# Kernel tuning notes

Measured on AMD Instinct MI355X. Metric: run time of the kernel, lower is better.

Reference implementation:

```python
import jax, jax.numpy as jnp
import numpy as np

# __init__ hyperparameters (defaults)
TRACE_BINS = 24
SMOOTH_KERNEL = 5
PAUSE_ENERGY_STD = -0.5
PAUSE_DELTA_Q = 0.35
VOICED_STD = -0.1
BOUNDARY_Q = 0.75

B, T, MEL = 64, 8000, 80


def _sliding_mean(x, k):
    """avg_pool1d(stride=1, padding=k//2, count_include_pad=True) via cumsum. x: [B,T]."""
    pad = k // 2
    xp = jnp.pad(x, ((0, 0), (pad, pad)))
    c = jnp.pad(jnp.cumsum(xp, axis=1), ((0, 0), (1, 0)))
    return (c[:, k:] - c[:, :-k]) / k


def _run_mean(mask):
    """Mean length of runs of True in mask [B,T] = (#ones)/(#runs), 0 if no runs."""
    prev_off = jnp.pad(~mask[:, :-1], ((0, 0), (1, 0)), constant_values=True)
    starts = mask & prev_off
    n_runs = starts.sum(axis=1).astype(jnp.float32)
    ones = mask.sum(axis=1).astype(jnp.float32)
    return jnp.where(n_runs > 0, ones / jnp.maximum(n_runs, 1.0), 0.0)


def setup_inputs() -> dict:
    key = jax.random.key(0)
    ref_mel = jax.random.normal(key, (B, T, MEL), dtype=jnp.float32)
    return {"ref_mel": ref_mel}


def reference(ref_mel):
    b, t, _ = ref_mel.shape
    energy = ref_mel.mean(axis=-1)                                  # [B,T]
    mu = energy.mean(axis=1, keepdims=True)
    sd = jnp.maximum(energy.std(axis=1, keepdims=True, ddof=1), 1e-6)  # torch.std is unbiased
    z = (energy - mu) / sd

    delta = jnp.pad(jnp.abs(energy[:, 1:] - energy[:, :-1]), ((0, 0), (1, 0)))
    dthr = jnp.quantile(delta, PAUSE_DELTA_Q, axis=1, keepdims=True)
    pause = (z <= PAUSE_ENERGY_STD) & (delta <= dthr)
    speech = ~pause
    voiced = (z > VOICED_STD).astype(jnp.float32)

    k = min(SMOOTH_KERNEL, max(1, t))
    local_rate = _sliding_mean(delta, k)[:, :t]
    k2 = min(k + 2, max(1, t))
    boundary_strength = _sliding_mean(delta, k2)[:, :t]

    sp = jnp.cumsum(speech.astype(jnp.float32), axis=1)
    total = jnp.maximum(sp[:, -1:], 1.0)
    progress = sp / total                                           # [B,T], nondecreasing
    uniform = jnp.linspace(0.0, 1.0, t)[None, :]
    seg_bias = progress - uniform

    bthr = jnp.quantile(boundary_strength, BOUNDARY_Q, axis=1, keepdims=True)
    bev = (boundary_strength >= bthr).astype(jnp.float32)

    feat = jnp.stack([pause.astype(jnp.float32), local_rate, bev, seg_bias, voiced], axis=-1)  # [B,T,5]

    # progress-based resampling: parallel binary search + gather + lerp
    target = jnp.linspace(0.0, 1.0, TRACE_BINS)
    right = jax.vmap(lambda p: jnp.searchsorted(p, target, side='left'))(progress)  # [B,bins]
    left = jnp.clip(right - 1, 0, t - 1)
    rc = jnp.clip(right, 0, t - 1)
    pl = jnp.take_along_axis(progress, left, axis=1)
    pr = jnp.take_along_axis(progress, rc, axis=1)
    denom = jnp.maximum(jnp.abs(pr - pl), 1e-6)
    alpha = jnp.clip((target[None, :] - pl) / denom, 0.0, 1.0)
    alpha = jnp.where(right <= 0, 0.0, jnp.where(right >= t, 1.0, alpha))[..., None]  # [B,bins,1]
    fdim = feat.shape[-1]
    li = jnp.broadcast_to(left[:, :, None], (b, TRACE_BINS, fdim))
    ri = jnp.broadcast_to(rc[:, :, None], (b, TRACE_BINS, fdim))
    fl = jnp.take_along_axis(feat, li, axis=1)
    fr = jnp.take_along_axis(feat, ri, axis=1)
    trace = fl * (1.0 - alpha) + fr * alpha                          # [B,bins,5]

    stats = jnp.stack([
        pause.astype(jnp.float32).mean(axis=1),
        _run_mean(pause),
        _run_mean(speech),
        local_rate[:, -1] - local_rate[:, 0],
        bev.mean(axis=1),
        voiced.mean(axis=1),
    ], axis=-1)                                                      # [B,6]
    return stats, trace
```

## Files before the change

### kernel.cpp

```cpp
#include <hip/hip_runtime.h>
#include <hip/hip_bf16.h>

#define TT 8000
#define BB 64
#define NBINS 24
#define CAP 256
#define NT 1024
#define NS 8
#define NHB 1024

__global__ __launch_bounds__(256) void k_energy(const float* __restrict__ mel,
                                                double* __restrict__ e_bt){
  __shared__ float sm[5120];
  const int blk = blockIdx.x, tid = threadIdx.x;
  const float4* g = (const float4*)(mel + (size_t)blk * 5120);
  float4* s4 = (float4*)sm;
  #pragma unroll
  for (int j = 0; j < 5; ++j) s4[tid + j * 256] = g[tid + j * 256];
  __syncthreads();
  const float* p = sm + tid * 20;
  double s = 0.0;
  #pragma unroll
  for (int j = 0; j < 20; ++j) s += (double)p[j];
  s += __shfl_xor(s, 1, 64);
  s += __shfl_xor(s, 2, 64);
  if ((tid & 3) == 0) e_bt[(size_t)blk * 64 + (tid >> 2)] = s / 80.0;
}

#define FALLBACK(VALS, RNK, OUTLO, MAXV, CBASE)                                  \
  {                                                                              \
    double lo_ = -0.5, hi_ = (MAXV);                                             \
    int cl_ = 0, ch_ = 8000;                                                     \
    for (;;){                                                                    \
      if (ch_ - cl_ <= CAP){                                                     \
        if (tid == 0) redI[0] = 0;                                               \
        __syncthreads();                                                         \
        _Pragma("unroll")                                                        \
        for (int s = 0; s < NS; ++s){                                            \
          int t = tid + (s << 10);                                               \
          if (t < TT){ double v = VALS[s];                                       \
            if (v > lo_ && v <= hi_){ int ix = atomicAdd(&redI[0], 1);           \
              if (ix < CAP) cand[(CBASE) + ix] = v; } }                          \
        }                                                                        \
        __syncthreads();                                                         \
        int n = redI[0]; if (n > CAP) n = CAP;                                   \
        int tgt = (RNK) - cl_;                                                   \
        if (tid < n){                                                            \
          double mv = cand[(CBASE) + tid];                                       \
          int rk = 0;                                                            \
          for (int j = 0; j < n; ++j){ double cj = cand[(CBASE) + j];            \
            rk += (cj < mv || (cj == mv && j < tid)) ? 1 : 0; }                  \
          if (rk == tgt)     scD[OUTLO] = mv;                                    \
          if (rk == tgt + 1) scD[(OUTLO) + 1] = mv;                              \
        }                                                                        \
        __syncthreads();                                                         \
        break;                                                                   \
      }                                                                          \
      double mid_ = 0.5 * (lo_ + hi_);                                           \
      if (!(mid_ > lo_ && mid_ < hi_)){                                          \
        if (tid == 0){ scD[OUTLO] = hi_; scD[(OUTLO) + 1] = hi_; }               \
        __syncthreads();                                                         \
        break;                                                                   \
      }                                                                          \
      int c_ = 0;                                                                \
      _Pragma("unroll")                                                          \
      for (int s = 0; s < NS; ++s){                                              \
        int t = tid + (s << 10);                                                 \
        if (t < TT && VALS[s] <= mid_) c_++;                                     \
      }                                                                          \
      _Pragma("unroll")                                                          \
      for (int o = 32; o; o >>= 1) c_ += __shfl_down(c_, o, 64);                 \
      if (lane == 0) redI[wid] = c_;                                             \
      __syncthreads();                                                           \
      if (tid == 0){ int a2 = 0; for (int i = 0; i < 16; ++i) a2 += redI[i]; scI[5] = a2; } \
      __syncthreads();                                                           \
      int ct_ = scI[5];                                                          \
      if (ct_ <= (RNK)){ lo_ = mid_; cl_ = ct_; }                                \
      else if (ct_ >= (RNK) + 2){ hi_ = mid_; ch_ = ct_; }                       \
      else {                                                                     \
        double mx_ = -1.0, mn_ = 1e300;                                          \
        _Pragma("unroll")                                                        \
        for (int s = 0; s < NS; ++s){                                            \
          int t = tid + (s << 10);                                               \
          if (t < TT){ double v = VALS[s];                                       \
            if (v <= mid_){ if (v > mx_) mx_ = v; } else { if (v < mn_) mn_ = v; } } \
        }                                                                        \
        _Pragma("unroll")                                                        \
        for (int o = 32; o; o >>= 1){ double x = __shfl_down(mx_, o, 64); if (x > mx_) mx_ = x; } \
        if (lane == 0) redD[wid] = mx_;                                          \
        __syncthreads();                                                         \
        if (tid == 0){ double a2 = redD[0]; for (int i = 1; i < 16; ++i) if (redD[i] > a2) a2 = redD[i]; scD[OUTLO] = a2; } \
        __syncthreads();                                                         \
        _Pragma("unroll")                                                        \
        for (int o = 32; o; o >>= 1){ double x = __shfl_down(mn_, o, 64); if (x < mn_) mn_ = x; } \
        if (lane == 0) redD[wid] = mn_;                                          \
        __syncthreads();                                                         \
        if (tid == 0){ double a2 = redD[0]; for (int i = 1; i < 16; ++i) if (redD[i] < a2) a2 = redD[i]; scD[(OUTLO) + 1] = a2; } \
        __syncthreads();                                                         \
        break;                                                                   \
      }                                                                          \
    }                                                                            \
  }

__global__ __launch_bounds__(NT) void k_row(const double* __restrict__ e_all,
                                            float* __restrict__ out){
  __shared__ double e_s[TT];
  __shared__ double delta_s[TT];
  __shared__ __align__(16) unsigned short runs[TT];
  __shared__ unsigned char flags[TT];
  __shared__ double cand[2 * CAP];
  __shared__ double redD[64];
  __shared__ int    redI[16];
  __shared__ double scD[12];
  __shared__ int    scI[16];
  __shared__ int    wTD[16], wOD[16], wTB[16], wOB[16], wT[16], wO[16];
  __shared__ int    cnt5[5];
  int* histD = (int*)runs;
  int* histB = histD + NHB;

  const int b = blockIdx.x, tid = threadIdx.x;
  const int lane = tid & 63, wid = tid >> 6;
  const double* eg = e_all + (size_t)b * TT;

  if (tid < 5) cnt5[tid] = 0;
  if (tid < 16) scI[tid] = 0;
  histD[tid] = 0; histB[tid] = 0;

  double ev[NS], dv[NS], bv[NS];
  #pragma unroll
  for (int s = 0; s < NS; ++s){
    int t = tid + (s << 10);
    double e = (t < TT) ? eg[t] : 0.0;
    ev[s] = e;
    if (t < TT) e_s[t] = e;
  }
  __syncthreads();
  #pragma unroll
  for (int s = 0; s < NS; ++s){
    int t = tid + (s << 10);
    double d = 0.0;
    if (t > 0 && t < TT) d = fabs(e_s[t] - e_s[t-1]);
    dv[s] = d;
    if (t < TT) delta_s[t] = d;
  }
  __syncthreads();
  #pragma unroll
  for (int s = 0; s < NS; ++s){
    int t = tid + (s << 10);
    double sum = 0.0;
    if (t < TT){
      int j0 = t - 3; if (j0 < 0) j0 = 0;
      int j1 = t + 3; if (j1 > TT-1) j1 = TT-1;
      for (int j = j0; j <= j1; ++j) sum += delta_s[j];
    }
    bv[s] = sum / 7.0;
  }
  {
    double se = 0.0, s2 = 0.0, md = 0.0, mb = 0.0;
    #pragma unroll
    for (int s = 0; s < NS; ++s){
      se += ev[s]; s2 += ev[s] * ev[s];
      if (dv[s] > md) md = dv[s];
      if (bv[s] > mb) mb = bv[s];
    }
    #pragma unroll
    for (int o = 32; o; o >>= 1){
      se += __shfl_down(se, o, 64);
      s2 += __shfl_down(s2, o, 64);
      double x = __shfl_down(md, o, 64); if (x > md) md = x;
      x = __shfl_down(mb, o, 64); if (x > mb) mb = x;
    }
    if (lane == 0){ redD[wid] = se; redD[16+wid] = s2; redD[32+wid] = md; redD[48+wid] = mb; }
  }
  __syncthreads();
  if (tid < 64){
    double a = (lane < 16) ? redD[lane]      : 0.0;
    double q = (lane < 16) ? redD[16 + lane] : 0.0;
    double c = (lane < 16) ? redD[32 + lane] : 0.0;
    double d = (lane < 16) ? redD[48 + lane] : 0.0;
    #pragma unroll
    for (int o = 8; o; o >>= 1){
      a += __shfl_down(a, o, 64);
      q += __shfl_down(q, o, 64);
      double x = __shfl_down(c, o, 64); if (x > c) c = x;
      x = __shfl_down(d, o, 64); if (x > d) d = x;
    }
    if (lane == 0){
      double mu0 = a / 8000.0;
      double var = (q - a * a / 8000.0) / 7999.0;
      if (var < 0.0) var = 0.0;
      double sd0 = sqrt(var); if (sd0 < 1e-6) sd0 = 1e-6;
      scD[0] = mu0; scD[1] = sd0; scD[9] = c; scD[10] = d;
    }
  }
  __syncthreads();
  const double mu = scD[0], sd = scD[1];
  const double maxd = scD[9], maxb = scD[10];
  const bool doD = (maxd > 0.0), doB = (maxb > 0.0);
  const double sclD = doD ? (double)NHB / maxd : 0.0;
  const double sclB = doB ? (double)NHB / maxb : 0.0;
  #pragma unroll
  for (int s = 0; s < NS; ++s){
    int t = tid + (s << 10);
    if (t < TT){
      if (doD){ int bi = (int)(dv[s] * sclD); if (bi > NHB-1) bi = NHB-1; atomicAdd(&histD[bi], 1); }
      if (doB){ int bi = (int)(bv[s] * sclB); if (bi > NHB-1) bi = NHB-1; atomicAdd(&histB[bi], 1); }
    }
  }
  __syncthreads();
  const int hD = histD[tid], hB = histB[tid];
  int incD = hD, incB = hB;
  #pragma unroll
  for (int o = 1; o < 64; o <<= 1){
    int x = __shfl_up(incD, o, 64); if (lane >= o) incD += x;
    x = __shfl_up(incB, o, 64); if (lane >= o) incB += x;
  }
  if (lane == 63){ wTD[wid] = incD; wTB[wid] = incB; }
  __syncthreads();
  if (tid < 64){
    int vD = (lane < 16) ? wTD[lane] : 0;
    int vB = (lane < 16) ? wTB[lane] : 0;
    int iD = vD, iB = vB;
    #pragma unroll
    for (int o = 1; o < 16; o <<= 1){
      int x = __shfl_up(iD, o, 64); if (lane >= o) iD += x;
      x = __shfl_up(iB, o, 64); if (lane >= o) iB += x;
    }
    if (lane < 16){ wOD[lane] = iD - vD; wOB[lane] = iB - vB; }
  }
  __syncthreads();
  {
    int PD = wOD[wid] + incD;
    int PB = wOB[wid] + incB;
    if (doD){
      if (2799 >= PD - hD && 2799 < PD){ scI[0] = tid; scI[2] = PD - hD; }
      if (2800 >= PD - hD && 2800 < PD){ scI[1] = tid; scI[3] = PD; }
    }
    if (doB){
      if (5999 >= PB - hB && 5999 < PB){ scI[8]  = tid; scI[10] = PB - hB; }
      if (6000 >= PB - hB && 6000 < PB){ scI[9]  = tid; scI[11] = PB; }
    }
  }
  __syncthreads();
  const int binrD = scI[0], binr1D = scI[1], PmD = scI[2], cwinD = scI[3] - scI[2];
  const int binrB = scI[8], binr1B = scI[9], PmB = scI[10], cwinB = scI[11] - scI[10];
  const bool fastD = doD && (cwinD <= CAP);
  const bool fastB = doB && (cwinB <= CAP);
  #pragma unroll
  for (int s = 0; s < NS; ++s){
    int t = tid + (s << 10);
    if (t < TT){
      if (fastD){
        int bi = (int)(dv[s] * sclD); if (bi > NHB-1) bi = NHB-1;
        if (bi >= binrD && bi <= binr1D){ int ix = atomicAdd(&scI[4], 1); if (ix < CAP) cand[ix] = dv[s]; }
      }
      if (fastB){
        int bi = (int)(bv[s] * sclB); if (bi > NHB-1) bi = NHB-1;
        if (bi >= binrB && bi <= binr1B){ int ix = atomicAdd(&scI[12], 1); if (ix < CAP) cand[CAP + ix] = bv[s]; }
      }
    }
  }
  __syncthreads();
  if (fastD){
    int n = scI[4]; if (n > CAP) n = CAP;
    int tgt = 2799 - PmD;
    if (tid < n){
      double mv = cand[tid];
      int rk = 0;
      for (int j = 0; j < n; ++j){ double cj = cand[j]; rk += (cj < mv || (cj == mv && j < tid)) ? 1 : 0; }
      if (rk == tgt)     scD[4] = mv;
      if (rk == tgt + 1) scD[5] = mv;
    }
  }
  if (fastB){
    int n = scI[12]; if (n > CAP) n = CAP;
    int tgt = 5999 - PmB;
    if (tid < n){
      double mv = cand[CAP + tid];
      int rk = 0;
      for (int j = 0; j < n; ++j){ double cj = cand[CAP + j]; rk += (cj < mv || (cj == mv && j < tid)) ? 1 : 0; }
      if (rk == tgt)     scD[6] = mv;
      if (rk == tgt + 1) scD[7] = mv;
    }
  }
  __syncthreads();
  if (doD && !fastD){ FALLBACK(dv, 2799, 4, maxd, 0) }
  if (doB && !fastB){ FALLBACK(bv, 5999, 6, maxb, CAP) }
  if (tid == 0){
    double gD = 0.35 * 7999.0 - 2799.0;
    double dd = scD[5] - scD[4];
    scD[2] = doD ? ((gD >= 0.5) ? (scD[5] - dd * (1.0 - gD)) : (scD[4] + dd * gD)) : 0.0;
    double gB = 0.75 * 7999.0 - 5999.0;
    double db = scD[7] - scD[6];
    scD[3] = doB ? ((gB >= 0.5) ? (scD[7] - db * (1.0 - gB)) : (scD[6] + db * gB)) : 0.0;
  }
  __syncthreads();
  const double dthr = scD[2], bthr = scD[3];
  #pragma unroll
  for (int s = 0; s < NS; ++s){
    int t = tid + (s << 10);
    if (t < TT){
      double z = (ev[s] - mu) / sd;
      bool pause  = (z <= -0.5) && (dv[s] <= dthr);
      bool voiced = (z > -0.1);
      bool bev    = (bv[s] >= bthr);
      flags[t] = (unsigned char)((pause ? 1 : 0) | (voiced ? 2 : 0) | (bev ? 4 : 0));
    }
  }
  __syncthreads();
  {
    int cp = 0, crp = 0, crs = 0, cv = 0, cb = 0;
    #pragma unroll
    for (int s = 0; s < NS; ++s){
      int t = tid + (s << 10);
      if (t < TT){
        unsigned f = flags[t];
        bool pause = (f & 1) != 0;
        bool prevP = (t > 0) ? ((flags[t-1] & 1) != 0) : false;
        cp += pause ? 1 : 0; cv += (f >> 1) & 1; cb += (f >> 2) & 1;
        if (pause && (t == 0 || !prevP)) crp++;
        if (!pause && (t == 0 || prevP)) crs++;
      }
    }
    #pragma unroll
    for (int o = 32; o; o >>= 1){
      cp += __shfl_down(cp, o, 64); crp += __shfl_down(crp, o, 64);
      crs += __shfl_down(crs, o, 64); cv += __shfl_down(cv, o, 64);
      cb += __shfl_down(cb, o, 64);
    }
    if (lane == 0){
      atomicAdd(&cnt5[0], cp); atomicAdd(&cnt5[1], crp); atomicAdd(&cnt5[2], crs);
      atomicAdd(&cnt5[3], cv); atomicAdd(&cnt5[4], cb);
    }
  }
  const int t0 = tid * 8;
  int ls = 0;
  if (t0 < TT){
    #pragma unroll
    for (int k = 0; k < 8; ++k) ls += (flags[t0 + k] & 1) ? 0 : 1;
  }
  int inc = ls;
  #pragma unroll
  for (int o = 1; o < 64; o <<= 1){ int x = __shfl_up(inc, o, 64); if (lane >= o) inc += x; }
  if (lane == 63) wT[wid] = inc;
  __syncthreads();
  if (tid < 64){
    int v = (lane < 16) ? wT[lane] : 0;
    int i2 = v;
    #pragma unroll
    for (int o = 1; o < 16; o <<= 1){ int x = __shfl_up(i2, o, 64); if (lane >= o) i2 += x; }
    if (lane < 16) wO[lane] = i2 - v;
    if (lane == 15) scD[8] = (i2 > 1) ? (double)i2 : 1.0;
  }
  __syncthreads();
  const double tf = scD[8];
  if (t0 < TT){
    int run = wO[wid] + (inc - ls);
    #pragma unroll
    for (int k = 0; k < 8; ++k){
      int t = t0 + k;
      run += (flags[t] & 1) ? 0 : 1;
      runs[t] = (unsigned short)run;
    }
  }
  __syncthreads();
  if (tid == 0){
    float onesP = (float)cnt5[0];
    float onesS = (float)(TT - cnt5[0]);
    float* st = out + b * 6;
    st[0] = onesP / 8000.0f;
    st[1] = (cnt5[1] > 0) ? (onesP / fmaxf((float)cnt5[1], 1.0f)) : 0.0f;
    st[2] = (cnt5[2] > 0) ? (onesS / fmaxf((float)cnt5[2], 1.0f)) : 0.0f;
    st[3] = (float)((delta_s[7997] + delta_s[7998] + delta_s[7999]) / 5.0
                  - (delta_s[0] + delta_s[1] + delta_s[2]) / 5.0);
    st[4] = ((float)cnt5[4]) / 8000.0f;
    st[5] = ((float)cnt5[3]) / 8000.0f;
  }
  if (tid < NBINS){
    double target = (tid == NBINS - 1) ? 1.0 : (double)tid * (1.0 / 23.0);
    int lo2 = 0, hi2 = TT;
    while (lo2 < hi2){
      int mid = (lo2 + hi2) >> 1;
      if ((double)runs[mid] / tf < target) lo2 = mid + 1; else hi2 = mid;
    }
    int right = lo2;
    int li = right - 1; if (li < 0) li = 0; if (li > TT-1) li = TT-1;
    int ri = right;     if (ri < 0) ri = 0; if (ri > TT-1) ri = TT-1;
    double pl = (double)runs[li] / tf, pr = (double)runs[ri] / tf;
    double denom = fabs(pr - pl); if (denom < 1e-6) denom = 1e-6;
    double alpha = (target - pl) / denom;
    if (alpha < 0.0) alpha = 0.0;
    if (alpha > 1.0) alpha = 1.0;
    if (right <= 0) alpha = 0.0;
    else if (right >= TT) alpha = 1.0;
    double fL[5], fR[5];
    for (int sdx = 0; sdx < 2; ++sdx){
      int i = sdx ? ri : li;
      double* f = sdx ? fR : fL;
      unsigned fl = flags[i];
      int j0 = i - 2; if (j0 < 0) j0 = 0;
      int j1 = i + 2; if (j1 > TT-1) j1 = TT-1;
      double ws = 0.0;
      for (int j = j0; j <= j1; ++j) ws += delta_s[j];
      f[0] = (fl & 1) ? 1.0 : 0.0;
      f[1] = ws / 5.0;
      f[2] = (fl & 4) ? 1.0 : 0.0;
      double u = (i == TT - 1) ? 1.0 : (double)i * (1.0 / 7999.0);
      f[3] = (double)runs[i] / tf - u;
      f[4] = (fl & 2) ? 1.0 : 0.0;
    }
    double om = 1.0 - alpha;
    float* tr = out + BB * 6 + ((size_t)b * NBINS + tid) * 5;
    #pragma unroll
    for (int f = 0; f < 5; ++f)
      tr[f] = (float)(fL[f] * om + fR[f] * alpha);
  }
}

extern "C" void kernel_launch(void* const* d_in, const int* in_sizes, int n_in,
                              void* d_out, int out_size, void* d_ws, size_t ws_size,
                              hipStream_t stream){
  const float* mel = (const float*)d_in[0];
  float* out = (float*)d_out;
  double* e_bt = (double*)d_ws;

  hipLaunchKernelGGL(k_energy, dim3(8000), dim3(256), 0, stream, mel, e_bt);
  hipLaunchKernelGGL(k_row,    dim3(BB),   dim3(NT),  0, stream, e_bt, out);
}
```

Baseline: 51.70 us.

## Use fixed histogram scale and cut block barriers in per-row quantile kernel

Replaces the data-dependent histogram scale, which needed a block-wide max reduction and barrier first, with a fixed scale of 1024. This lets histogram building run in the same pass as the mean/variance accumulation. Several __syncthreads and small scan stages are removed: neighbour deltas come from wavefront shuffles, previous-pause flags come from bitmasks, and per-wave prefix offsets are summed redundantly by each thread. The risk is that a fixed scale clusters values into few bins, which would push more rows into the slower fallback selection path (that path now computes its own max).

Measured after the change: 51.22 us, median of 2. No clear change (-0.9%).

```diff
diff --git a/kernel.cpp b/kernel.cpp
--- a/kernel.cpp
+++ b/kernel.cpp
@@ -8,6 +8,7 @@
 #define NT 1024
 #define NS 8
 #define NHB 1024
+#define FSCALE 1024.0
 
 __global__ __launch_bounds__(256) void k_energy(const float* __restrict__ mel,
                                                 double* __restrict__ e_bt){
@@ -27,9 +28,21 @@
   if ((tid & 3) == 0) e_bt[(size_t)blk * 64 + (tid >> 2)] = s / 80.0;
 }
 
-#define FALLBACK(VALS, RNK, OUTLO, MAXV, CBASE)                                  \
+#define FALLBACK(VALS, RNK, OUTLO, CBASE)                                        \
   {                                                                              \
-    double lo_ = -0.5, hi_ = (MAXV);                                             \
+    double mx0 = 0.0;                                                            \
+    _Pragma("unroll")                                                            \
+    for (int s = 0; s < NS; ++s){                                                \
+      int t = tid + (s << 10);                                                   \
+      if (t < TT && VALS[s] > mx0) mx0 = VALS[s];                                \
+    }                                                                            \
+    _Pragma("unroll")                                                            \
+    for (int o = 32; o; o >>= 1){ double x = __shfl_down(mx0, o, 64); if (x > mx0) mx0 = x; } \
+    if (lane == 0) redD[wid] = mx0;                                              \
+    __syncthreads();                                                             \
+    if (tid == 0){ double a2 = redD[0]; for (int i = 1; i < 16; ++i) if (redD[i] > a2) a2 = redD[i]; scD[11] = a2; } \
+    __syncthreads();                                                             \
+    double lo_ = -0.5, hi_ = scD[11];                                            \
     int cl_ = 0, ch_ = 8000;                                                     \
     for (;;){                                                                    \
       if (ch_ - cl_ <= CAP){                                                     \
@@ -109,11 +122,11 @@
   __shared__ __align__(16) unsigned short runs[TT];
   __shared__ unsigned char flags[TT];
   __shared__ double cand[2 * CAP];
-  __shared__ double redD[64];
+  __shared__ double redD[32];
   __shared__ int    redI[16];
   __shared__ double scD[12];
   __shared__ int    scI[16];
-  __shared__ int    wTD[16], wOD[16], wTB[16], wOB[16], wT[16], wO[16];
+  __shared__ int    wTD[16], wTB[16], wT[16];
   __shared__ int    cnt5[5];
   int* histD = (int*)runs;
   int* histB = histD + NHB;
@@ -134,128 +147,87 @@
     ev[s] = e;
     if (t < TT) e_s[t] = e;
   }
-  __syncthreads();
   #pragma unroll
   for (int s = 0; s < NS; ++s){
     int t = tid + (s << 10);
-    double d = 0.0;
-    if (t > 0 && t < TT) d = fabs(e_s[t] - e_s[t-1]);
+    double ep = __shfl_up(ev[s], 1, 64);
+    if (lane == 0 && t > 0 && t < TT) ep = eg[t - 1];
+    double d = (t > 0 && t < TT) ? fabs(ev[s] - ep) : 0.0;
     dv[s] = d;
     if (t < TT) delta_s[t] = d;
   }
   __syncthreads();
-  #pragma unroll
-  for (int s = 0; s < NS; ++s){
-    int t = tid + (s << 10);
-    double sum = 0.0;
-    if (t < TT){
-      int j0 = t - 3; if (j0 < 0) j0 = 0;
-      int j1 = t + 3; if (j1 > TT-1) j1 = TT-1;
-      for (int j = j0; j <= j1; ++j) sum += delta_s[j];
-    }
-    bv[s] = sum / 7.0;
-  }
   {
-    double se = 0.0, s2 = 0.0, md = 0.0, mb = 0.0;
+    double se = 0.0, s2 = 0.0;
     #pragma unroll
     for (int s = 0; s < NS; ++s){
-      se += ev[s]; s2 += ev[s] * ev[s];
-      if (dv[s] > md) md = dv[s];
-      if (bv[s] > mb) mb = bv[s];
-    }
-    #pragma unroll
-    for (int o = 32; o; o >>= 1){
-      se += __shfl_down(se, o, 64);
-      s2 += __shfl_down(s2, o, 64);
-      double x = __shfl_down(md, o, 64); if (x > md) md = x;
-      x = __shfl_down(mb, o, 64); if (x > mb) mb = x;
-    }
-    if (lane == 0){ redD[wid] = se; redD[16+wid] = s2; redD[32+wid] = md; redD[48+wid] = mb; }
-  }
-  __syncthreads();
+      int t = tid + (s << 10);
+      double bw = 0.0;
+      if (t < TT){
+        int j0 = t - 3; if (j0 < 0) j0 = 0;
+        int j1 = t + 3; if (j1 > TT - 1) j1 = TT - 1;
+        double sum = 0.0;
+        for (int j = j0; j <= j1; ++j) sum += delta_s[j];
+        bw = sum / 7.0;
+        int biD = (int)(dv[s] * FSCALE); if (biD > NHB - 1) biD = NHB - 1;
+        atomicAdd(&histD[biD], 1);
+        int biB = (int)(bw * FSCALE); if (biB > NHB - 1) biB = NHB - 1;
+        atomicAdd(&histB[biB], 1);
+        se += ev[s]; s2 += ev[s] * ev[s];
+      }
+      bv[s] = bw;
+    }
+    #pragma unroll
+    for (int o = 32; o; o >>= 1){ se += __shfl_down(se, o, 64); s2 += __shfl_down(s2, o, 64); }
+    if (lane == 0){ redD[wid] = se; redD[16 + wid] = s2; }
+  }
+  __syncthreads();
+  const int hD = histD[tid], hB = histB[tid];
+  int incD = hD, incB = hB;
+  #pragma unroll
+  for (int o = 1; o < 64; o <<= 1){
+    int x = __shfl_up(incD, o, 64); if (lane >= o) incD += x;
+    x = __shfl_up(incB, o, 64); if (lane >= o) incB += x;
+  }
+  if (lane == 63){ wTD[wid] = incD; wTB[wid] = incB; }
   if (tid < 64){
-    double a = (lane < 16) ? redD[lane]      : 0.0;
+    double a = (lane < 16) ? redD[lane] : 0.0;
     double q = (lane < 16) ? redD[16 + lane] : 0.0;
-    double c = (lane < 16) ? redD[32 + lane] : 0.0;
-    double d = (lane < 16) ? redD[48 + lane] : 0.0;
-    #pragma unroll
-    for (int o = 8; o; o >>= 1){
-      a += __shfl_down(a, o, 64);
-      q += __shfl_down(q, o, 64);
-      double x = __shfl_down(c, o, 64); if (x > c) c = x;
-      x = __shfl_down(d, o, 64); if (x > d) d = x;
-    }
+    #pragma unroll
+    for (int o = 8; o; o >>= 1){ a += __shfl_down(a, o, 64); q += __shfl_down(q, o, 64); }
     if (lane == 0){
       double mu0 = a / 8000.0;
       double var = (q - a * a / 8000.0) / 7999.0;
       if (var < 0.0) var = 0.0;
       double sd0 = sqrt(var); if (sd0 < 1e-6) sd0 = 1e-6;
-      scD[0] = mu0; scD[1] = sd0; scD[9] = c; scD[10] = d;
-    }
-  }
-  __syncthreads();
-  const double mu = scD[0], sd = scD[1];
-  const double maxd = scD[9], maxb = scD[10];
-  const bool doD = (maxd > 0.0), doB = (maxb > 0.0);
-  const double sclD = doD ? (double)NHB / maxd : 0.0;
-  const double sclB = doB ? (double)NHB / maxb : 0.0;
-  #pragma unroll
-  for (int s = 0; s < NS; ++s){
-    int t = tid + (s << 10);
-    if (t < TT){
-      if (doD){ int bi = (int)(dv[s] * sclD); if (bi > NHB-1) bi = NHB-1; atomicAdd(&histD[bi], 1); }
-      if (doB){ int bi = (int)(bv[s] * sclB); if (bi > NHB-1) bi = NHB-1; atomicAdd(&histB[bi], 1); }
-    }
-  }
-  __syncthreads();
-  const int hD = histD[tid], hB = histB[tid];
-  int incD = hD, incB = hB;
-  #pragma unroll
-  for (int o = 1; o < 64; o <<= 1){
-    int x = __shfl_up(incD, o, 64); if (lane >= o) incD += x;
-    x = __shfl_up(incB, o, 64); if (lane >= o) incB += x;
-  }
-  if (lane == 63){ wTD[wid] = incD; wTB[wid] = incB; }
-  __syncthreads();
-  if (tid < 64){
-    int vD = (lane < 16) ? wTD[lane] : 0;
-    int vB = (lane < 16) ? wTB[lane] : 0;
-    int iD = vD, iB = vB;
-    #pragma unroll
-    for (int o = 1; o < 16; o <<= 1){
-      int x = __shfl_up(iD, o, 64); if (lane >= o) iD += x;
-      x = __shfl_up(iB, o, 64); if (lane >= o) iB += x;
-    }
-    if (lane < 16){ wOD[lane] = iD - vD; wOB[lane] = iB - vB; }
+      scD[0] = mu0; scD[1] = sd0;
+    }
   }
   __syncthreads();
   {
-    int PD = wOD[wid] + incD;
-    int PB = wOB[wid] + incB;
-    if (doD){
-      if (2799 >= PD - hD && 2799 < PD){ scI[0] = tid; scI[2] = PD - hD; }
-      if (2800 >= PD - hD && 2800 < PD){ scI[1] = tid; scI[3] = PD; }
-    }
-    if (doB){
-      if (5999 >= PB - hB && 5999 < PB){ scI[8]  = tid; scI[10] = PB - hB; }
-      if (6000 >= PB - hB && 6000 < PB){ scI[9]  = tid; scI[11] = PB; }
-    }
+    int preD = 0, preB = 0;
+    #pragma unroll
+    for (int i = 0; i < 16; ++i){ if (i < wid){ preD += wTD[i]; preB += wTB[i]; } }
+    int PD = preD + incD, PB = preB + incB;
+    if (2799 >= PD - hD && 2799 < PD){ scI[0] = tid; scI[2] = PD - hD; }
+    if (2800 >= PD - hD && 2800 < PD){ scI[1] = tid; scI[3] = PD; }
+    if (5999 >= PB - hB && 5999 < PB){ scI[8]  = tid; scI[10] = PB - hB; }
+    if (6000 >= PB - hB && 6000 < PB){ scI[9]  = tid; scI[11] = PB; }
   }
   __syncthreads();
   const int binrD = scI[0], binr1D = scI[1], PmD = scI[2], cwinD = scI[3] - scI[2];
   const int binrB = scI[8], binr1B = scI[9], PmB = scI[10], cwinB = scI[11] - scI[10];
-  const bool fastD = doD && (cwinD <= CAP);
-  const bool fastB = doB && (cwinB <= CAP);
+  const bool fastD = (cwinD <= CAP), fastB = (cwinB <= CAP);
   #pragma unroll
   for (int s = 0; s < NS; ++s){
     int t = tid + (s << 10);
     if (t < TT){
       if (fastD){
-        int bi = (int)(dv[s] * sclD); if (bi > NHB-1) bi = NHB-1;
+        int bi = (int)(dv[s] * FSCALE); if (bi > NHB - 1) bi = NHB - 1;
         if (bi >= binrD && bi <= binr1D){ int ix = atomicAdd(&scI[4], 1); if (ix < CAP) cand[ix] = dv[s]; }
       }
       if (fastB){
-        int bi = (int)(bv[s] * sclB); if (bi > NHB-1) bi = NHB-1;
+        int bi = (int)(bv[s] * FSCALE); if (bi > NHB - 1) bi = NHB - 1;
         if (bi >= binrB && bi <= binr1B){ int ix = atomicAdd(&scI[12], 1); if (ix < CAP) cand[CAP + ix] = bv[s]; }
       }
     }
@@ -284,18 +256,16 @@
     }
   }
   __syncthreads();
-  if (doD && !fastD){ FALLBACK(dv, 2799, 4, maxd, 0) }
-  if (doB && !fastB){ FALLBACK(bv, 5999, 6, maxb, CAP) }
-  if (tid == 0){
-    double gD = 0.35 * 7999.0 - 2799.0;
-    double dd = scD[5] - scD[4];
-    scD[2] = doD ? ((gD >= 0.5) ? (scD[5] - dd * (1.0 - gD)) : (scD[4] + dd * gD)) : 0.0;
-    double gB = 0.75 * 7999.0 - 5999.0;
-    double db = scD[7] - scD[6];
-    scD[3] = doB ? ((gB >= 0.5) ? (scD[7] - db * (1.0 - gB)) : (scD[6] + db * gB)) : 0.0;
-  }
-  __syncthreads();
-  const double dthr = scD[2], bthr = scD[3];
+  if (!fastD){ FALLBACK(dv, 2799, 4, 0) }
+  if (!fastB){ FALLBACK(bv, 5999, 6, CAP) }
+  const double mu = scD[0], sd = scD[1];
+  const double gD = 0.35 * 7999.0 - 2799.0;
+  const double dd = scD[5] - scD[4];
+  const double dthr = (gD >= 0.5) ? (scD[5] - dd * (1.0 - gD)) : (scD[4] + dd * gD);
+  const double gB = 0.75 * 7999.0 - 5999.0;
+  const double db = scD[7] - scD[6];
+  const double bthr = (gB >= 0.5) ? (scD[7] - db * (1.0 - gB)) : (scD[6] + db * gB);
+  unsigned pmask = 0, vmask = 0, bmask = 0;
   #pragma unroll
   for (int s = 0; s < NS; ++s){
     int t = tid + (s << 10);
@@ -304,20 +274,28 @@
       bool pause  = (z <= -0.5) && (dv[s] <= dthr);
       bool voiced = (z > -0.1);
       bool bev    = (bv[s] >= bthr);
+      if (pause)  pmask |= 1u << s;
+      if (voiced) vmask |= 1u << s;
+      if (bev)    bmask |= 1u << s;
       flags[t] = (unsigned char)((pause ? 1 : 0) | (voiced ? 2 : 0) | (bev ? 4 : 0));
     }
   }
-  __syncthreads();
   {
+    unsigned pprev = __shfl_up(pmask, 1, 64);
     int cp = 0, crp = 0, crs = 0, cv = 0, cb = 0;
     #pragma unroll
     for (int s = 0; s < NS; ++s){
       int t = tid + (s << 10);
       if (t < TT){
-        unsigned f = flags[t];
-        bool pause = (f & 1) != 0;
-        bool prevP = (t > 0) ? ((flags[t-1] & 1) != 0) : false;
-        cp += pause ? 1 : 0; cv += (f >> 1) & 1; cb += (f >> 2) & 1;
+        bool pause = (pmask >> s) & 1;
+        cp += (pmask >> s) & 1; cv += (vmask >> s) & 1; cb += (bmask >> s) & 1;
+        bool prevP = false;
+        if (t > 0){
+          if (lane == 0){
+            double zp = (e_s[t - 1] - mu) / sd;
+            prevP = (zp <= -0.5) && (delta_s[t - 1] <= dthr);
+          } else prevP = (pprev >> s) & 1;
+        }
         if (pause && (t == 0 || !prevP)) crp++;
         if (!pause && (t == 0 || prevP)) crs++;
       }
@@ -333,6 +311,7 @@
       atomicAdd(&cnt5[3], cv); atomicAdd(&cnt5[4], cb);
     }
   }
+  __syncthreads();
   const int t0 = tid * 8;
   int ls = 0;
   if (t0 < TT){
@@ -343,27 +322,6 @@
   #pragma unroll
   for (int o = 1; o < 64; o <<= 1){ int x = __shfl_up(inc, o, 64); if (lane >= o) inc += x; }
   if (lane == 63) wT[wid] = inc;
-  __syncthreads();
-  if (tid < 64){
-    int v = (lane < 16) ? wT[lane] : 0;
-    int i2 = v;
-    #pragma unroll
-    for (int o = 1; o < 16; o <<= 1){ int x = __shfl_up(i2, o, 64); if (lane >= o) i2 += x; }
-    if (lane < 16) wO[lane] = i2 - v;
-    if (lane == 15) scD[8] = (i2 > 1) ? (double)i2 : 1.0;
-  }
-  __syncthreads();
-  const double tf = scD[8];
-  if (t0 < TT){
-    int run = wO[wid] + (inc - ls);
-    #pragma unroll
-    for (int k = 0; k < 8; ++k){
-      int t = t0 + k;
-      run += (flags[t] & 1) ? 0 : 1;
-      runs[t] = (unsigned short)run;
-    }
-  }
-  __syncthreads();
   if (tid == 0){
     float onesP = (float)cnt5[0];
     float onesS = (float)(TT - cnt5[0]);
@@ -376,6 +334,21 @@
     st[4] = ((float)cnt5[4]) / 8000.0f;
     st[5] = ((float)cnt5[3]) / 8000.0f;
   }
+  __syncthreads();
+  int totAll = 0, pre = 0;
+  #pragma unroll
+  for (int i = 0; i < 16; ++i){ int v = wT[i]; totAll += v; if (i < wid) pre += v; }
+  const double tf = (totAll > 1) ? (double)totAll : 1.0;
+  if (t0 < TT){
+    int run = pre + (inc - ls);
+    #pragma unroll
+    for (int k = 0; k < 8; ++k){
+      int t = t0 + k;
+      run += (flags[t] & 1) ? 0 : 1;
+      runs[t] = (unsigned short)run;
+    }
+  }
+  __syncthreads();
   if (tid < NBINS){
     double target = (tid == NBINS - 1) ? 1.0 : (double)tid * (1.0 / 23.0);
     int lo2 = 0, hi2 = TT;
@@ -384,8 +357,8 @@
       if ((double)runs[mid] / tf < target) lo2 = mid + 1; else hi2 = mid;
     }
     int right = lo2;
-    int li = right - 1; if (li < 0) li = 0; if (li > TT-1) li = TT-1;
-    int ri = right;     if (ri < 0) ri = 0; if (ri > TT-1) ri = TT-1;
+    int li = right - 1; if (li < 0) li = 0; if (li > TT - 1) li = TT - 1;
+    int ri = right;     if (ri < 0) ri = 0; if (ri > TT - 1) ri = TT - 1;
     double pl = (double)runs[li] / tf, pr = (double)runs[ri] / tf;
     double denom = fabs(pr - pl); if (denom < 1e-6) denom = 1e-6;
     double alpha = (target - pl) / denom;
@@ -399,7 +372,7 @@
       double* f = sdx ? fR : fL;
       unsigned fl = flags[i];
       int j0 = i - 2; if (j0 < 0) j0 = 0;
-      int j1 = i + 2; if (j1 > TT-1) j1 = TT-1;
+      int j1 = i + 2; if (j1 > TT - 1) j1 = TT - 1;
       double ws = 0.0;
       for (int j = j0; j <= j1; ++j) ws += delta_s[j];
       f[0] = (fl & 1) ? 1.0 : 0.0;
```
